# Kernel tuning notes

Hardware: AMD Instinct MI355X
Metric: run time of the kernel (lower is better)

The kernel has to match this reference:

```python
import jax, jax.numpy as jnp
jax.config.update("jax_enable_x64", True)
import numpy as np

B, S, BITS = 1024, 4096, 32
_SHIFTS = jnp.arange(31, -1, -1, dtype=jnp.uint32)  # bit 0 = MSB


def _decode_fp32(bits):
    """[..., 32] {0,1} pulses -> float32 values (bitwise-exact)."""
    u = jnp.sum(bits.astype(jnp.uint32) << _SHIFTS, axis=-1, dtype=jnp.uint32)
    return jax.lax.bitcast_convert_type(u, jnp.float32)


def _encode_fp32(vals):
    """float32 values -> [..., 32] {0,1} pulses (bitwise-exact)."""
    u = jax.lax.bitcast_convert_type(vals, jnp.uint32)
    return ((u[..., None] >> _SHIFTS) & jnp.uint32(1)).astype(jnp.float32)


def _gelu_exact_fp64(x32):
    """Mirror of the spiking pipeline: fp32->fp64, exact tanh-GELU in fp64
    using tanh(z) = (exp(2z)-1)/(exp(2z)+1), then round back to fp32."""
    x = x32.astype(jnp.float64)                      # FP32ToFP64Converter
    x_cubed = (x * x) * x                            # two fp64 muls
    inner = x + 0.044715 * x_cubed                   # adder + mul
    two_z = 2.0 * (0.7978845608028654 * inner)       # two muls
    e = jnp.exp(two_z)                               # fp64 exp
    tanh = (e - 1.0) / (e + 1.0)                     # adders + divider
    y = 0.5 * (x * (1.0 + tanh))                     # adder + two muls
    return y.astype(jnp.float32)                     # FP64ToFP32Converter


def setup_inputs() -> dict:
    key = jax.random.key(0)
    # Generate realistic pre-activation values and bit-expand to pulses so the
    # [..., 32] pulse tensor encodes valid IEEE-754 float32 patterns.
    vals = jax.random.normal(key, (B, S), dtype=jnp.float32) * 2.0
    return {"x": _encode_fp32(vals)}


def reference(x) -> jnp.ndarray:
    # x: [B, S, 32] pulse bits -> GELU(x) as [B, S, 32] pulse bits
    return _encode_fp32(_gelu_exact_fp64(_decode_fp32(x)))
```

## Files before the change

kernel.cpp:

```cpp
#include <hip/hip_runtime.h>
#include <cmath>


__global__ __launch_bounds__(256) void spike_gelu_kernel(
    const float4* __restrict__ in, float4* __restrict__ out, long n4) {
  long f = (long)blockIdx.x * (long)blockDim.x + (long)threadIdx.x;
  if (f >= n4) return;

  float4 p = in[f];

  unsigned g = (unsigned)threadIdx.x & 7u;
  unsigned nib = ((p.x != 0.0f) ? 8u : 0u) | ((p.y != 0.0f) ? 4u : 0u) |
                 ((p.z != 0.0f) ? 2u : 0u) | ((p.w != 0.0f) ? 1u : 0u);
  unsigned s = 28u - 4u * g;
  unsigned u = nib << s;

  u |= __shfl_xor(u, 1, 8);
  u |= __shfl_xor(u, 2, 8);
  u |= __shfl_xor(u, 4, 8);

  float xf = __uint_as_float(u);

  double y;
  {
#pragma clang fp contract(off)
    double x = (double)xf;
    double x_cubed = (x * x) * x;
    double inner = x + 0.044715 * x_cubed;
    double two_z = 2.0 * (0.7978845608028654 * inner);
    double e = exp(two_z);
    double th = (e - 1.0) / (e + 1.0);
    y = 0.5 * (x * (1.0 + th));
  }
  float yf = (float)y;

  unsigned r = __float_as_uint(yf);
  float4 o;
  o.x = (float)((r >> (s + 3u)) & 1u);
  o.y = (float)((r >> (s + 2u)) & 1u);
  o.z = (float)((r >> (s + 1u)) & 1u);
  o.w = (float)((r >> s) & 1u);
  out[f] = o;
}

extern "C" void kernel_launch(void* const* d_in, const int* in_sizes, int n_in,
                              void* d_out, int out_size, void* d_ws, size_t ws_size,
                              hipStream_t stream) {
  const float4* in = (const float4*)d_in[0];
  float4* out = (float4*)d_out;
  long n4 = (long)in_sizes[0] / 4;
  int block = 256;
  long grid = (n4 + block - 1) / block;
  spike_gelu_kernel<<<(int)grid, block, 0, stream>>>(in, out, n4);
}
```

Before: 803.4 us.

## Give each lane one unique float's GELU instead of eight redundant copies

Previously the eight lanes holding one float's 32 pulse bits each evaluated the full fp64 GELU, exp included, so the work ran eight times over. Now each wavefront handles 512 float4s: it loads eight coalesced rounds and keeps one assembled word per lane, runs the fp64 math once per lane, then redistributes result bits with wave shuffles for eight coalesced stores. Pulses are read by testing exponent bit 23 rather than a float compare, which is valid only because pulses are exactly 0.0 or 1.0. The cost is extra shuffles, a longer unrolled loop and more registers per thread. The launch assumes n4 is a multiple of 512, and there is no per-element bounds check.

```diff
diff --git a/kernel.cpp b/kernel.cpp
--- a/kernel.cpp
+++ b/kernel.cpp
@@ -4,23 +4,31 @@
 
 __global__ __launch_bounds__(256) void spike_gelu_kernel(
     const float4* __restrict__ in, float4* __restrict__ out, long n4) {
-  long f = (long)blockIdx.x * (long)blockDim.x + (long)threadIdx.x;
-  if (f >= n4) return;
+  const int lane = (int)(threadIdx.x & 63u);
+  const long wid = (long)blockIdx.x * (blockDim.x >> 6) + (threadIdx.x >> 6);
+  const long base = wid * 512;
+  if (base >= n4) return;
 
-  float4 p = in[f];
+  const unsigned g = (unsigned)lane & 7u;
+  const unsigned k = (unsigned)lane >> 3;
+  const unsigned s = 28u - 4u * g;
 
-  unsigned g = (unsigned)threadIdx.x & 7u;
-  unsigned nib = ((p.x != 0.0f) ? 8u : 0u) | ((p.y != 0.0f) ? 4u : 0u) |
-                 ((p.z != 0.0f) ? 2u : 0u) | ((p.w != 0.0f) ? 1u : 0u);
-  unsigned s = 28u - 4u * g;
-  unsigned u = nib << s;
+  unsigned myword = 0u;
+#pragma unroll
+  for (int j = 0; j < 8; ++j) {
+    float4 p = in[base + (long)(j * 64 + lane)];
+    unsigned nib = (((__float_as_uint(p.x) >> 23) & 1u) << 3) |
+                   (((__float_as_uint(p.y) >> 23) & 1u) << 2) |
+                   (((__float_as_uint(p.z) >> 23) & 1u) << 1) |
+                   (((__float_as_uint(p.w) >> 23) & 1u));
+    unsigned u = nib << s;
+    u |= __shfl_xor(u, 1, 8);
+    u |= __shfl_xor(u, 2, 8);
+    u |= __shfl_xor(u, 4, 8);
+    if ((int)g == j) myword = u;
+  }
 
-  u |= __shfl_xor(u, 1, 8);
-  u |= __shfl_xor(u, 2, 8);
-  u |= __shfl_xor(u, 4, 8);
-
-  float xf = __uint_as_float(u);
-
+  float xf = __uint_as_float(myword);
   double y;
   {
 #pragma clang fp contract(off)
@@ -33,14 +41,18 @@
     y = 0.5 * (x * (1.0 + th));
   }
   float yf = (float)y;
+  unsigned r = __float_as_uint(yf);
 
-  unsigned r = __float_as_uint(yf);
-  float4 o;
-  o.x = (float)((r >> (s + 3u)) & 1u);
-  o.y = (float)((r >> (s + 2u)) & 1u);
-  o.z = (float)((r >> (s + 1u)) & 1u);
-  o.w = (float)((r >> s) & 1u);
-  out[f] = o;
+#pragma unroll
+  for (int j = 0; j < 8; ++j) {
+    unsigned w = __shfl((int)r, (int)(k * 8u + (unsigned)j), 64);
+    float4 o;
+    o.x = (float)((w >> (s + 3u)) & 1u);
+    o.y = (float)((w >> (s + 2u)) & 1u);
+    o.z = (float)((w >> (s + 1u)) & 1u);
+    o.w = (float)((w >> s) & 1u);
+    out[base + (long)(j * 64 + lane)] = o;
+  }
 }
 
 extern "C" void kernel_launch(void* const* d_in, const int* in_sizes, int n_in,
@@ -49,7 +61,7 @@
   const float4* in = (const float4*)d_in[0];
   float4* out = (float4*)d_out;
   long n4 = (long)in_sizes[0] / 4;
-  int block = 256;
-  long grid = (n4 + block - 1) / block;
+  const int block = 256;
+  long grid = (n4 + 2048 - 1) / 2048;
   spike_gelu_kernel<<<(int)grid, block, 0, stream>>>(in, out, n4);
 }
```

Result: slower. 835.2 us (+4.0%).
